# Kernel tuning notes

Measured on AMD Instinct MI355X. Metric: run time of the kernel, lower is better.

The kernel has to match this reference:

```python
import math
import jax, jax.numpy as jnp
import numpy as np

L, H, K, NH, V, DFF = 6, 512, 512, 8, 64, 1024
B, T, S = 8, 512, 512
PAD = 0


def _ln(x, g, b, eps=1e-5):
    m = jnp.mean(x, -1, keepdims=True)
    v = jnp.mean((x - m) ** 2, -1, keepdims=True)
    return (x - m) * jax.lax.rsqrt(v + eps) * g + b


def _mha(Q, Kin, Vin, mask, wq, bq, wk, bk, wv, bv, wo, bo, g, b):
    # weights stored [in, out]
    B_, Tq, Hd = Q.shape
    dk = wq.shape[1] // NH
    dv = wv.shape[1] // NH
    q = (Q @ wq + bq).reshape(B_, Tq, NH, dk).transpose(0, 2, 1, 3)
    k = (Kin @ wk + bk).reshape(B_, -1, NH, dk).transpose(0, 2, 1, 3)
    v = (Vin @ wv + bv).reshape(B_, -1, NH, dv).transpose(0, 2, 1, 3)
    scores = jnp.einsum('bhqd,bhkd->bhqk', q, k) / jnp.sqrt(jnp.float32(dk))
    scores = jnp.where(mask[:, None, :, :], jnp.float32(-1e9), scores)
    attn = jax.nn.softmax(scores, axis=-1)
    ctx = jnp.einsum('bhqk,bhkd->bhqd', attn, v).transpose(0, 2, 1, 3).reshape(B_, Tq, Hd)
    return _ln(ctx @ wo + bo + Q, g, b)


def _pe(t, d):
    pos = jnp.arange(t, dtype=jnp.float32)[:, None]
    div = jnp.exp(jnp.arange(0, d, 2, dtype=jnp.float32) * (-math.log(10000.0) / d))
    pe = jnp.zeros((t, d), jnp.float32)
    pe = pe.at[:, 0::2].set(jnp.sin(pos * div)).at[:, 1::2].set(jnp.cos(pos * div))
    return pe


def setup_inputs() -> dict:
    key = jax.random.key(0)
    ks = iter(jax.random.split(key, 40))
    nrm = lambda shape, s=0.02: jax.random.normal(next(ks), shape, jnp.float32) * s
    inp = {
        'smiles_index': jax.random.randint(next(ks), (B, T), 0, V, dtype=jnp.int32),
        'enc_outputs': jax.random.normal(next(ks), (B, S, H), jnp.float32),
        'enc_pad_mask': jnp.zeros((B, 1, S), bool),
        'tgt_len': T,
        'mol_emb': nrm((V, H), 1.0).at[PAD].set(0.0),  # padding_idx=0 row zeroed
        # self-attn stacks [L, ...]
        'sa_wq': nrm((L, H, K)), 'sa_bq': jnp.zeros((L, K)),
        'sa_wk': nrm((L, H, K)), 'sa_bk': jnp.zeros((L, K)),
        'sa_wv': nrm((L, H, H)), 'sa_bv': jnp.zeros((L, H)),
        'sa_wo': nrm((L, H, H)), 'sa_bo': jnp.zeros((L, H)),
        'ln1_g': jnp.ones((L, H)), 'ln1_b': jnp.zeros((L, H)),
        # cross-attn stacks
        'ea_wq': nrm((L, H, K)), 'ea_bq': jnp.zeros((L, K)),
        'ea_wk': nrm((L, H, K)), 'ea_bk': jnp.zeros((L, K)),
        'ea_wv': nrm((L, H, H)), 'ea_bv': jnp.zeros((L, H)),
        'ea_wo': nrm((L, H, H)), 'ea_bo': jnp.zeros((L, H)),
        'ln2_g': jnp.ones((L, H)), 'ln2_b': jnp.zeros((L, H)),
        # conv1x1 FFN == per-position linear
        'c1_w': nrm((L, H, DFF)), 'c1_b': jnp.zeros((L, DFF)),
        'c2_w': nrm((L, DFF, H)), 'c2_b': jnp.zeros((L, H)),
        'ln3_g': jnp.ones((L, H)), 'ln3_b': jnp.zeros((L, H)),
    }
    return inp


def reference(smiles_index, enc_outputs, enc_pad_mask, tgt_len, mol_emb,
              sa_wq, sa_bq, sa_wk, sa_bk, sa_wv, sa_bv, sa_wo, sa_bo, ln1_g, ln1_b,
              ea_wq, ea_bq, ea_wk, ea_bk, ea_wv, ea_bv, ea_wo, ea_bo, ln2_g, ln2_b,
              c1_w, c1_b, c2_w, c2_b, ln3_g, ln3_b):
    b, t = smiles_index.shape
    s = enc_outputs.shape[1]
    # embeddings + sinusoidal positional encoding (dropout is identity in eval)
    x = mol_emb[smiles_index] + _pe(t, mol_emb.shape[1])[None]
    # masks: pad (key == pad_id) OR causal upper-triangular
    pad = (smiles_index == PAD)[:, None, :]                 # [B,1,T] -> broadcast over queries
    causal = jnp.triu(jnp.ones((t, t), bool), 1)[None]      # [1,T,T]
    self_mask = pad | causal                                # [B,T,T]
    enc_mask = jnp.broadcast_to(enc_pad_mask, (b, t, s))    # [B,T,S]
    for l in range(L):
        x = _mha(x, x, x, self_mask,
                 sa_wq[l], sa_bq[l], sa_wk[l], sa_bk[l], sa_wv[l], sa_bv[l],
                 sa_wo[l], sa_bo[l], ln1_g[l], ln1_b[l])
        x = _mha(x, enc_outputs, enc_outputs, enc_mask,
                 ea_wq[l], ea_bq[l], ea_wk[l], ea_bk[l], ea_wv[l], ea_bv[l],
                 ea_wo[l], ea_bo[l], ln2_g[l], ln2_b[l])
        h = jax.nn.relu(x @ c1_w[l] + c1_b[l])
        y = h @ c2_w[l] + c2_b[l]
        x = _ln(y + x, ln3_g[l], ln3_b[l])
    return x
```

## Files before the change

kernel.cpp:

```cpp
#include <hip/hip_runtime.h>
#include <hip/hip_bf16.h>
#include <math.h>

#define NL   6
#define HD   512
#define NHD  8
#define DK   64
#define DFFN 1024
#define NB   8
#define TT   512
#define MROWS (NB*TT)
#define SQC  262144

typedef __hip_bfloat16 bf16;
typedef __attribute__((ext_vector_type(8))) short short8v;
typedef __attribute__((ext_vector_type(4))) short short4v;
typedef __attribute__((ext_vector_type(4))) float f32x4;

__device__ __forceinline__ float wave_sum(float v) {
#pragma unroll
  for (int off = 32; off; off >>= 1) v += __shfl_xor(v, off);
  return v;
}
__device__ __forceinline__ unsigned short f2bf(float x) {
  __hip_bfloat16 h = __float2bfloat16(x);
  return *reinterpret_cast<unsigned short*>(&h);
}

struct Srcs8 { const float* s[8]; };
__global__ __launch_bounds__(256)
void wprep8_kernel(Srcs8 srcs, bf16* __restrict__ wt) {
  const int z = blockIdx.z;
  const int which = z & 7, l = z >> 3;
  const long long baseT[8] = {0, 0, 0, 18LL*SQC, 24LL*SQC, 30LL*SQC, 30LL*SQC, 42LL*SQC};
  const long long lstrT[8] = {3LL*SQC, 3LL*SQC, 3LL*SQC, SQC, SQC, 2LL*SQC, 2LL*SQC, SQC};
  const int rowOffT[8] = {0, 512, 1024, 0, 0, 0, 512, 0};

  __shared__ float t[32][33];
  const float* W = srcs.s[which] + (size_t)l * SQC;
  bf16* dst = wt + baseT[which] + (size_t)l * lstrT[which] + (size_t)rowOffT[which] * HD;
  const int n0 = blockIdx.x * 32, k0 = blockIdx.y * 32;
  const int tx = threadIdx.x & 31, ty = threadIdx.x >> 5;
#pragma unroll
  for (int j = 0; j < 4; ++j)
    t[ty + j * 8][tx] = W[(size_t)(k0 + ty + j * 8) * HD + n0 + tx];
  __syncthreads();
#pragma unroll
  for (int j = 0; j < 4; ++j)
    dst[(size_t)(n0 + ty + j * 8) * HD + k0 + tx] = __float2bfloat16(t[tx][ty + j * 8]);
}

__global__ __launch_bounds__(256)
void wprep_kernel(const float* __restrict__ W, bf16* __restrict__ Wt, int Kd, int Nd) {
  __shared__ float t[32][33];
  const size_t src = (size_t)blockIdx.z * Kd * Nd;
  const int n0 = blockIdx.x * 32, k0 = blockIdx.y * 32;
  const int tx = threadIdx.x & 31, ty = threadIdx.x >> 5;
#pragma unroll
  for (int j = 0; j < 4; ++j)
    t[ty + j * 8][tx] = W[src + (size_t)(k0 + ty + j * 8) * Nd + n0 + tx];
  __syncthreads();
#pragma unroll
  for (int j = 0; j < 4; ++j)
    Wt[src + (size_t)(n0 + ty + j * 8) * Kd + k0 + tx] = __float2bfloat16(t[tx][ty + j * 8]);
}

__global__ __launch_bounds__(256)
void bcat2_kernel(const float* __restrict__ b0, const float* __restrict__ b1,
                  const float* __restrict__ b2, const float* __restrict__ c0,
                  const float* __restrict__ c1, float* __restrict__ outS,
                  float* __restrict__ outKV) {
  const int l = blockIdx.x;
  if (blockIdx.y == 0) {
    for (int i = threadIdx.x; i < 1536; i += 256) {
      const int seg = i >> 9, off = i & 511;
      const float* src = seg == 0 ? b0 : (seg == 1 ? b1 : b2);
      outS[(size_t)l * 1536 + i] = src[(size_t)l * 512 + off];
    }
  } else {
    for (int i = threadIdx.x; i < 1024; i += 256) {
      const float* src = (i >> 9) == 0 ? c0 : c1;
      outKV[(size_t)l * 1024 + i] = src[(size_t)l * 512 + (i & 511)];
    }
  }
}

__global__ __launch_bounds__(256)
void cvtbf16_kernel(const float* __restrict__ in, unsigned short* __restrict__ out) {
  const int i = (blockIdx.x * 256 + threadIdx.x) * 4;
  float4 v = *(const float4*)(in + i);
  out[i + 0] = f2bf(v.x); out[i + 1] = f2bf(v.y);
  out[i + 2] = f2bf(v.z); out[i + 3] = f2bf(v.w);
}

__global__ __launch_bounds__(256)
void embed_pe_kernel(const int* __restrict__ idx, const float* __restrict__ emb,
                     float* __restrict__ x, unsigned short* __restrict__ xb) {
  const int row = blockIdx.x;
  const int t = row & (TT - 1);
  const int tok = idx[row];
  const float cdiv = -0.017988946009466842f;
#pragma unroll
  for (int e0 = 0; e0 < 2; ++e0) {
    const int e = threadIdx.x + e0 * 256;
    const float div = __expf((float)(e & ~1) * cdiv);
    const float ang = (float)t * div;
    const float pe = (e & 1) ? cosf(ang) : sinf(ang);
    const float v = emb[(size_t)tok * HD + e] + pe;
    x[(size_t)row * HD + e] = v;
    xb[(size_t)row * HD + e] = f2bf(v);
  }
}

__device__ __forceinline__ void gemm_compute(const char* As, const char* Bs,
                                             int wm, int wn, int lane,
                                             f32x4 (&acc)[2][2]) {
  const int rsw = (lane & 7) << 4;
  const int csel = (lane >> 4) * 16;
  short8v af[2][2], bfr[2][2];
#pragma unroll
  for (int m = 0; m < 2; ++m)
#pragma unroll
    for (int kk = 0; kk < 2; ++kk) {
      const int row = wm * 32 + m * 16 + (lane & 15);
      af[m][kk] = *(const short8v*)(As + row * 128 + ((kk * 64 + csel) ^ rsw));
    }
#pragma unroll
  for (int n = 0; n < 2; ++n)
#pragma unroll
    for (int kk = 0; kk < 2; ++kk) {
      const int row = wn * 32 + n * 16 + (lane & 15);
      bfr[n][kk] = *(const short8v*)(Bs + row * 128 + ((kk * 64 + csel) ^ rsw));
    }
#pragma unroll
  for (int m = 0; m < 2; ++m)
#pragma unroll
    for (int n = 0; n < 2; ++n) {
      acc[m][n] = __builtin_amdgcn_mfma_f32_16x16x32_bf16(af[m][0], bfr[n][0], acc[m][n], 0, 0, 0);
      acc[m][n] = __builtin_amdgcn_mfma_f32_16x16x32_bf16(af[m][1], bfr[n][1], acc[m][n], 0, 0, 0);
    }
}

template<int OUT_BF16, int RELU, int ADDRES>
__device__ __forceinline__
void mgemm_body(const bf16* __restrict__ A, const bf16* __restrict__ Bt,
                const float* __restrict__ bias, const float* __restrict__ res,
                float* __restrict__ Cf, unsigned short* __restrict__ Cb,
                int N, int K, int m0, int n0, char* As, char* Bs) {
  const int tid = threadIdx.x;
  const int w = tid >> 6, lane = tid & 63;
  const int wm = w >> 1, wn = w & 1;

  const int sr = w * 16 + (lane >> 3);
  const int scol = (lane & 7) * 16;
  const int swc = scol ^ ((sr & 7) << 4);
  const bf16* ga0 = A + (size_t)(m0 + sr) * K + (scol >> 1);
  const bf16* ga1 = A + (size_t)(m0 + sr + 8) * K + (scol >> 1);
  const bf16* gb0 = Bt + (size_t)(n0 + sr) * K + (scol >> 1);
  const bf16* gb1 = Bt + (size_t)(n0 + sr + 8) * K + (scol >> 1);
  char* la0 = As + sr * 128 + swc;
  char* la1 = As + (sr + 8) * 128 + swc;
  char* lb0 = Bs + sr * 128 + swc;
  char* lb1 = Bs + (sr + 8) * 128 + swc;

  f32x4 acc[2][2] = {};

  short8v ra0 = *(const short8v*)ga0, ra1 = *(const short8v*)ga1;
  short8v rb0 = *(const short8v*)gb0, rb1 = *(const short8v*)gb1;
  short8v sa0, sa1, sb0, sb1;

  for (int k0 = 0; k0 < K; k0 += 128) {
    __syncthreads();
    *(short8v*)la0 = ra0; *(short8v*)la1 = ra1;
    *(short8v*)lb0 = rb0; *(short8v*)lb1 = rb1;
    __syncthreads();
    sa0 = *(const short8v*)(ga0 + k0 + 64); sa1 = *(const short8v*)(ga1 + k0 + 64);
    sb0 = *(const short8v*)(gb0 + k0 + 64); sb1 = *(const short8v*)(gb1 + k0 + 64);
    gemm_compute(As, Bs, wm, wn, lane, acc);
    __syncthreads();
    *(short8v*)la0 = sa0; *(short8v*)la1 = sa1;
    *(short8v*)lb0 = sb0; *(short8v*)lb1 = sb1;
    __syncthreads();
    if (k0 + 128 < K) {
      ra0 = *(const short8v*)(ga0 + k0 + 128); ra1 = *(const short8v*)(ga1 + k0 + 128);
      rb0 = *(const short8v*)(gb0 + k0 + 128); rb1 = *(const short8v*)(gb1 + k0 + 128);
    }
    gemm_compute(As, Bs, wm, wn, lane, acc);
  }

  const int crow = (lane >> 4) * 4;
  const int ccol = lane & 15;
#pragma unroll
  for (int m = 0; m < 2; ++m)
#pragma unroll
    for (int n = 0; n < 2; ++n) {
      const int gr = m0 + wm * 32 + m * 16 + crow;
      const int gc = n0 + wn * 32 + n * 16 + ccol;
      const float bs = bias[gc];
#pragma unroll
      for (int r = 0; r < 4; ++r) {
        float v = acc[m][n][r] + bs;
        if (RELU) v = fmaxf(v, 0.f);
        if (ADDRES) v += res[(size_t)(gr + r) * N + gc];
        if (OUT_BF16) Cb[(size_t)(gr + r) * N + gc] = f2bf(v);
        else          Cf[(size_t)(gr + r) * N + gc] = v;
      }
    }
}

template<int OUT_BF16, int RELU, int ADDRES>
__global__ __launch_bounds__(256)
void mgemm_kernel(const bf16* __restrict__ A, const bf16* __restrict__ Bt,
                  const float* __restrict__ bias, const float* __restrict__ res,
                  float* __restrict__ Cf, unsigned short* __restrict__ Cb,
                  int N, int K) {
  __shared__ __attribute__((aligned(16))) char As[64 * 128];
  __shared__ __attribute__((aligned(16))) char Bs[64 * 128];
  mgemm_body<OUT_BF16, RELU, ADDRES>(A, Bt, bias, res, Cf, Cb, N, K,
                                     blockIdx.x * 64, blockIdx.y * 64, As, Bs);
}

__global__ __launch_bounds__(256)
void mgemm_cross_kernel(const bf16* __restrict__ A1, const bf16* __restrict__ B1,
                        const float* __restrict__ bias1, unsigned short* __restrict__ C1,
                        const bf16* __restrict__ A2, const bf16* __restrict__ B2,
                        const float* __restrict__ bias2, unsigned short* __restrict__ C2) {
  __shared__ __attribute__((aligned(16))) char As[64 * 128];
  __shared__ __attribute__((aligned(16))) char Bs[64 * 128];
  if (blockIdx.y < 8)
    mgemm_body<1, 0, 0>(A1, B1, bias1, nullptr, nullptr, C1, 512, 512,
                        blockIdx.x * 64, blockIdx.y * 64, As, Bs);
  else
    mgemm_body<1, 0, 0>(A2, B2, bias2, nullptr, nullptr, C2, 1024, 512,
                        blockIdx.x * 64, (blockIdx.y - 8) * 64, As, Bs);
}

template<int CAUSAL>
__global__ __launch_bounds__(512)
void mattn_kernel(const unsigned short* __restrict__ q, const unsigned short* __restrict__ kgl,
                  const unsigned short* __restrict__ vgl, unsigned short* __restrict__ ctx,
                  const int* __restrict__ idx, const unsigned char* __restrict__ emask,
                  int qstride, int kvstride) {
  __shared__ __attribute__((aligned(16))) unsigned short kt[64 * 64];
  __shared__ __attribute__((aligned(16))) unsigned short vt[64 * 64];
  __shared__ __attribute__((aligned(16))) unsigned short pl[8][16 * 64];
  __shared__ float km[64];

  const int bh = blockIdx.x;
  const int b = bh >> 3, h = bh & 7;
  const int tid = threadIdx.x, w = tid >> 6, lane = tid & 63;
  const int l4 = lane & 15, g = lane >> 4;

  int qb_w;
  if (CAUSAL) {
    const int strip = (w < 4) ? blockIdx.y : 7 - blockIdx.y;
    qb_w = strip * 64 + (w & 3) * 16;
  } else {
    qb_w = blockIdx.y * 128 + w * 16;
  }
  const int kvEnd = CAUSAL ? (8 - blockIdx.y) * 64 : TT;

  const unsigned short* qp = q + (size_t)(b * TT + qb_w + l4) * qstride + h * DK + g * 8;
  short8v aq0 = *(const short8v*)qp;
  short8v aq1 = *(const short8v*)(qp + 32);

  const int sr_k = tid >> 3, sc8 = tid & 7;
  const unsigned short* kbp = kgl + (size_t)(b * TT + sr_k) * kvstride + h * DK + sc8 * 8;
  const int k2 = (tid & 31) * 2, d4 = (tid >> 5) * 4;
  const unsigned short* vbp0 = vgl + (size_t)(b * TT + k2) * kvstride + h * DK + d4;
  const unsigned short* vbp1 = vbp0 + kvstride;

  short8v rk = *(const short8v*)kbp;
  short4v rv0 = *(const short4v*)vbp0;
  short4v rv1 = *(const short4v*)vbp1;
  float mreg = 0.f;
  if (tid < 64) {
    const int kp = b * TT + tid;
    mreg = (CAUSAL ? (idx[kp] == 0) : (emask[kp] != 0)) ? -1e9f : 0.f;
  }

  float m_r[4], l_r[4];
  f32x4 acc_o[4];
#pragma unroll
  for (int r = 0; r < 4; ++r) { m_r[r] = -1e30f; l_r[r] = 0.f; }
#pragma unroll
  for (int f = 0; f < 4; ++f) acc_o[f] = (f32x4){0.f, 0.f, 0.f, 0.f};

  for (int kt0 = 0; kt0 < kvEnd; kt0 += 64) {
    __syncthreads();
    if (tid < 64) km[tid] = mreg;
    *(short8v*)((char*)kt + sr_k * 128 + ((sc8 * 16) ^ ((sr_k & 7) << 4))) = rk;
#pragma unroll
    for (int j = 0; j < 4; ++j) {
      const int d = d4 + j;
      const unsigned pk = ((unsigned)(unsigned short)rv0[j]) | (((unsigned)(unsigned short)rv1[j]) << 16);
      *(unsigned*)((char*)vt + d * 128 + ((k2 * 2) ^ ((d & 7) << 4))) = pk;
    }
    __syncthreads();

    if (kt0 + 64 < kvEnd) {
      const size_t off = (size_t)(kt0 + 64) * kvstride;
      rk = *(const short8v*)(kbp + off);
      rv0 = *(const short4v*)(vbp0 + off);
      rv1 = *(const short4v*)(vbp1 + off);
      if (tid < 64) {
        const int kp = b * TT + kt0 + 64 + tid;
        mreg = (CAUSAL ? (idx[kp] == 0) : (emask[kp] != 0)) ? -1e9f : 0.f;
      }
    }

    if (!(CAUSAL && kt0 > qb_w + 15)) {
      const bool diag = CAUSAL && (kt0 + 64 > qb_w);

      f32x4 s4[4];
      __builtin_amdgcn_s_setprio(1);
#pragma unroll
      for (int f = 0; f < 4; ++f) {
        const int krow = f * 16 + l4;
        const int sw = (krow & 7) << 4;
        short8v bk0 = *(const short8v*)((const char*)kt + krow * 128 + ((g * 16) ^ sw));
        short8v bk1 = *(const short8v*)((const char*)kt + krow * 128 + ((64 + g * 16) ^ sw));
        f32x4 a = {};
        a = __builtin_amdgcn_mfma_f32_16x16x32_bf16(aq0, bk0, a, 0, 0, 0);
        a = __builtin_amdgcn_mfma_f32_16x16x32_bf16(aq1, bk1, a, 0, 0, 0);
        s4[f] = a;
      }
      __builtin_amdgcn_s_setprio(0);

      float kmb[4];
#pragma unroll
      for (int f = 0; f < 4; ++f) kmb[f] = km[f * 16 + l4];

      float sc_r[4];
#pragma unroll
      for (int r = 0; r < 4; ++r) {
        const int qpos = qb_w + g * 4 + r;
        float sf[4];
#pragma unroll
        for (int f = 0; f < 4; ++f) sf[f] = fmaf(s4[f][r], 0.125f, kmb[f]);
        if (diag) {
#pragma unroll
          for (int f = 0; f < 4; ++f) {
            const int kpos = kt0 + f * 16 + l4;
            sf[f] = (kpos > qpos) ? -1e9f : sf[f];
          }
        }
        float mx = fmaxf(fmaxf(sf[0], sf[1]), fmaxf(sf[2], sf[3]));
#pragma unroll
        for (int off = 8; off; off >>= 1) mx = fmaxf(mx, __shfl_xor(mx, off));
        const float mn = fmaxf(m_r[r], mx);
        const float sc = __expf(m_r[r] - mn);
        m_r[r] = mn;
        sc_r[r] = sc;
        float ps = 0.f;
        const int prow = g * 4 + r;
        const int psw = (prow & 7) << 4;
#pragma unroll
        for (int f = 0; f < 4; ++f) {
          const float p = __expf(sf[f] - mn);
          ps += p;
          *(unsigned short*)((char*)pl[w] + prow * 128 + ((f * 32 + l4 * 2) ^ psw)) = f2bf(p);
        }
#pragma unroll
        for (int off = 8; off; off >>= 1) ps += __shfl_xor(ps, off);
        l_r[r] = l_r[r] * sc + ps;
      }

#pragma unroll
      for (int f = 0; f < 4; ++f)
#pragma unroll
        for (int r = 0; r < 4; ++r) acc_o[f][r] *= sc_r[r];

      const int asw = (l4 & 7) << 4;
      short8v pa0 = *(const short8v*)((const char*)pl[w] + l4 * 128 + ((g * 16) ^ asw));
      short8v pa1 = *(const short8v*)((const char*)pl[w] + l4 * 128 + ((g * 16 + 64) ^ asw));
      __builtin_amdgcn_s_setprio(1);
#pragma unroll
      for (int f = 0; f < 4; ++f) {
        const int drow = f * 16 + l4;
        const int sw = (drow & 7) << 4;
        short8v vb0 = *(const short8v*)((const char*)vt + drow * 128 + ((g * 16) ^ sw));
        short8v vb1 = *(const short8v*)((const char*)vt + drow * 128 + ((g * 16 + 64) ^ sw));
        acc_o[f] = __builtin_amdgcn_mfma_f32_16x16x32_bf16(pa0, vb0, acc_o[f], 0, 0, 0);
        acc_o[f] = __builtin_amdgcn_mfma_f32_16x16x32_bf16(pa1, vb1, acc_o[f], 0, 0, 0);
      }
      __builtin_amdgcn_s_setprio(0);
    }
  }

  float rl[4];
#pragma unroll
  for (int r = 0; r < 4; ++r) rl[r] = 1.f / l_r[r];
#pragma unroll
  for (int f = 0; f < 4; ++f)
#pragma unroll
    for (int r = 0; r < 4; ++r) {
      const int row = qb_w + g * 4 + r;
      const int col = h * DK + f * 16 + l4;
      ctx[(size_t)(b * TT + row) * HD + col] = f2bf(acc_o[f][r] * rl[r]);
    }
}

__global__ __launch_bounds__(256)
void ln2_kernel(const float* __restrict__ v, float* __restrict__ out,
                unsigned short* __restrict__ outb,
                const float* __restrict__ g, const float* __restrict__ bta) {
  const int row = blockIdx.x;
  const int tid = threadIdx.x;
  const int w = tid >> 6, lane = tid & 63;
  const size_t ro = (size_t)row * HD;

  float v0 = v[ro + tid];
  float v1 = v[ro + tid + 256];

  __shared__ float red[4];
  float s = wave_sum(v0 + v1);
  if (lane == 0) red[w] = s;
  __syncthreads();
  const float mean = (red[0] + red[1] + red[2] + red[3]) * (1.f / HD);
  __syncthreads();

  const float d0 = v0 - mean, d1 = v1 - mean;
  float qv = wave_sum(d0 * d0 + d1 * d1);
  if (lane == 0) red[w] = qv;
  __syncthreads();
  const float var = (red[0] + red[1] + red[2] + red[3]) * (1.f / HD);
  const float rstd = rsqrtf(var + 1e-5f);

  const float o0 = d0 * rstd * g[tid] + bta[tid];
  const float o1 = d1 * rstd * g[tid + 256] + bta[tid + 256];
  out[ro + tid] = o0;
  out[ro + tid + 256] = o1;
  outb[ro + tid] = f2bf(o0);
  outb[ro + tid + 256] = f2bf(o1);
}

extern "C" void kernel_launch(void* const* d_in, const int* in_sizes, int n_in,
                              void* d_out, int out_size, void* d_ws, size_t ws_size,
                              hipStream_t stream) {
  const int* idx = (const int*)d_in[0];
  const float* enc = (const float*)d_in[1];
  const unsigned char* emask = (const unsigned char*)d_in[2];
  const float* emb = (const float*)d_in[4];
  const float* sa_wq = (const float*)d_in[5];
  const float* sa_bq = (const float*)d_in[6];
  const float* sa_wk = (const float*)d_in[7];
  const float* sa_bk = (const float*)d_in[8];
  const float* sa_wv = (const float*)d_in[9];
  const float* sa_bv = (const float*)d_in[10];
  const float* sa_wo = (const float*)d_in[11];
  const float* sa_bo = (const float*)d_in[12];
  const float* ln1g = (const float*)d_in[13];
  const float* ln1b = (const float*)d_in[14];
  const float* ea_wq = (const float*)d_in[15];
  const float* ea_bq = (const float*)d_in[16];
  const float* ea_wk = (const float*)d_in[17];
  const float* ea_bk = (const float*)d_in[18];
  const float* ea_wv = (const float*)d_in[19];
  const float* ea_bv = (const float*)d_in[20];
  const float* ea_wo = (const float*)d_in[21];
  const float* ea_bo = (const float*)d_in[22];
  const float* ln2g = (const float*)d_in[23];
  const float* ln2b = (const float*)d_in[24];
  const float* c1w = (const float*)d_in[25];
  const float* c1b = (const float*)d_in[26];
  const float* c2w = (const float*)d_in[27];
  const float* c2b = (const float*)d_in[28];
  const float* ln3g = (const float*)d_in[29];
  const float* ln3b = (const float*)d_in[30];

  const size_t MH = (size_t)MROWS * HD;
  const size_t SQ = (size_t)SQC;
  char* ws = (char*)d_ws;
  float*          x    = (float*)(ws + 0);
  unsigned short* xb   = (unsigned short*)(ws + (8u << 20));
  unsigned short* qkvb = (unsigned short*)(ws + (12u << 20));
  unsigned short* qcb  = (unsigned short*)(ws + (24u << 20));
  unsigned short* kvb  = (unsigned short*)(ws + (28u << 20));
  unsigned short* cxb  = (unsigned short*)(ws + (36u << 20));
  float*          yb   = (float*)(ws + (40u << 20));
  unsigned short* encb = (unsigned short*)(ws + (56u << 20));
  bf16*           wt   = (bf16*)(ws + (60u << 20));
  float*          bcS  = (float*)(ws + (98u << 20));
  float*          bcKV = (float*)(ws + (99u << 20));
  unsigned short* hb   = qkvb;

  bf16* t_saqkv = wt;
  bf16* t_sao   = wt + 18 * SQ;
  bf16* t_eaq   = wt + 24 * SQ;
  bf16* t_eakv  = wt + 30 * SQ;
  bf16* t_eao   = wt + 42 * SQ;
  bf16* t_c1    = wt + 48 * SQ;
  bf16* t_c2    = wt + 60 * SQ;

  const dim3 blk(256);
  const dim3 blk512(512);
  const dim3 gQKV(MROWS / 64, 1536 / 64);
  const dim3 g1024(MROWS / 64, 1024 / 64);
  const dim3 g512(MROWS / 64, 512 / 64);
  const dim3 gCross(MROWS / 64, 24);
  const dim3 attng(NB * NHD, 4);

  Srcs8 s8;
  s8.s[0] = sa_wq; s8.s[1] = sa_wk; s8.s[2] = sa_wv; s8.s[3] = sa_wo;
  s8.s[4] = ea_wq; s8.s[5] = ea_wk; s8.s[6] = ea_wv; s8.s[7] = ea_wo;
  wprep8_kernel<<<dim3(16, 16, 48), blk, 0, stream>>>(s8, wt);
  wprep_kernel<<<dim3(32, 16, NL), blk, 0, stream>>>(c1w, t_c1, HD, DFFN);
  wprep_kernel<<<dim3(16, 32, NL), blk, 0, stream>>>(c2w, t_c2, DFFN, HD);
  bcat2_kernel<<<dim3(NL, 2), blk, 0, stream>>>(sa_bq, sa_bk, sa_bv, ea_bk, ea_bv, bcS, bcKV);
  cvtbf16_kernel<<<MH / 1024, blk, 0, stream>>>(enc, encb);

  embed_pe_kernel<<<MROWS, blk, 0, stream>>>(idx, emb, x, xb);

  for (int l = 0; l < NL; ++l) {
    const size_t b512 = (size_t)l * HD;
    const size_t bFF = (size_t)l * DFFN;
    float* lnout = (l == NL - 1) ? (float*)d_out : x;

    mgemm_kernel<1, 0, 0><<<gQKV, blk, 0, stream>>>(
        (const bf16*)xb, t_saqkv + (size_t)l * 3 * SQ, bcS + (size_t)l * 1536,
        nullptr, nullptr, qkvb, 1536, HD);
    mattn_kernel<1><<<attng, blk512, 0, stream>>>(qkvb, qkvb + 512, qkvb + 1024, cxb,
                                                  idx, emask, 1536, 1536);
    mgemm_kernel<0, 0, 1><<<g512, blk, 0, stream>>>(
        (const bf16*)cxb, t_sao + (size_t)l * SQ, sa_bo + b512, x, yb, nullptr, HD, HD);
    ln2_kernel<<<MROWS, blk, 0, stream>>>(yb, x, xb, ln1g + b512, ln1b + b512);

    mgemm_cross_kernel<<<gCross, blk, 0, stream>>>(
        (const bf16*)xb, t_eaq + (size_t)l * SQ, ea_bq + b512, qcb,
        (const bf16*)encb, t_eakv + (size_t)l * 2 * SQ, bcKV + (size_t)l * 1024, kvb);
    mattn_kernel<0><<<attng, blk512, 0, stream>>>(qcb, kvb, kvb + 512, cxb,
                                                  idx, emask, 512, 1024);
    mgemm_kernel<0, 0, 1><<<g512, blk, 0, stream>>>(
        (const bf16*)cxb, t_eao + (size_t)l * SQ, ea_bo + b512, x, yb, nullptr, HD, HD);
    ln2_kernel<<<MROWS, blk, 0, stream>>>(yb, x, xb, ln2g + b512, ln2b + b512);

    mgemm_kernel<1, 1, 0><<<g1024, blk, 0, stream>>>(
        (const bf16*)xb, t_c1 + (size_t)l * 2 * SQ, c1b + bFF, nullptr, nullptr, hb, DFFN, HD);
    mgemm_kernel<0, 0, 1><<<g512, blk, 0, stream>>>(
        (const bf16*)hb, t_c2 + (size_t)l * 2 * SQ, c2b + b512, x, yb, nullptr, HD, DFFN);
    ln2_kernel<<<MROWS, blk, 0, stream>>>(yb, lnout, xb, ln3g + b512, ln3b + b512);
  }
}
```

Before: 825.2 us.

## Double-buffer LDS tiles in GEMM and attention, add XCD-aware block swizzle

The GEMM and attention kernels now use two LDS buffers for their tiles, which cuts each k-step to a single barrier instead of two. The next tile's global loads are issued before that barrier. Block indices are also remapped so consecutive tiles land on the same XCD, aiming for better L2 reuse across the chiplets. In exchange, LDS use doubles, which may lower occupancy. The swizzle assumes the grid size divides evenly by 8.

```diff
diff --git a/kernel.cpp b/kernel.cpp
--- a/kernel.cpp
+++ b/kernel.cpp
@@ -25,6 +25,13 @@
 __device__ __forceinline__ unsigned short f2bf(float x) {
   __hip_bfloat16 h = __float2bfloat16(x);
   return *reinterpret_cast<unsigned short*>(&h);
+}
+
+__device__ __forceinline__ void xcd_swz(int gy, int& mblk, int& nblk) {
+  const int raw = blockIdx.x * gy + blockIdx.y;
+  const int chunk = (gridDim.x * gy) >> 3;
+  const int swz = (raw & 7) * chunk + (raw >> 3);
+  mblk = swz / gy; nblk = swz % gy;
 }
 
 struct Srcs8 { const float* s[8]; };
@@ -158,34 +165,28 @@
   const bf16* ga1 = A + (size_t)(m0 + sr + 8) * K + (scol >> 1);
   const bf16* gb0 = Bt + (size_t)(n0 + sr) * K + (scol >> 1);
   const bf16* gb1 = Bt + (size_t)(n0 + sr + 8) * K + (scol >> 1);
-  char* la0 = As + sr * 128 + swc;
-  char* la1 = As + (sr + 8) * 128 + swc;
-  char* lb0 = Bs + sr * 128 + swc;
-  char* lb1 = Bs + (sr + 8) * 128 + swc;
 
   f32x4 acc[2][2] = {};
 
   short8v ra0 = *(const short8v*)ga0, ra1 = *(const short8v*)ga1;
   short8v rb0 = *(const short8v*)gb0, rb1 = *(const short8v*)gb1;
-  short8v sa0, sa1, sb0, sb1;
-
-  for (int k0 = 0; k0 < K; k0 += 128) {
+
+  const int NT = K >> 6;
+  for (int t = 0; t < NT; ++t) {
+    char* Ab = As + (t & 1) * 8192;
+    char* Bb = Bs + (t & 1) * 8192;
+    *(short8v*)(Ab + sr * 128 + swc) = ra0;
+    *(short8v*)(Ab + (sr + 8) * 128 + swc) = ra1;
+    *(short8v*)(Bb + sr * 128 + swc) = rb0;
+    *(short8v*)(Bb + (sr + 8) * 128 + swc) = rb1;
+    if (t + 1 < NT) {
+      ra0 = *(const short8v*)(ga0 + (t + 1) * 64);
+      ra1 = *(const short8v*)(ga1 + (t + 1) * 64);
+      rb0 = *(const short8v*)(gb0 + (t + 1) * 64);
+      rb1 = *(const short8v*)(gb1 + (t + 1) * 64);
+    }
     __syncthreads();
-    *(short8v*)la0 = ra0; *(short8v*)la1 = ra1;
-    *(short8v*)lb0 = rb0; *(short8v*)lb1 = rb1;
-    __syncthreads();
-    sa0 = *(const short8v*)(ga0 + k0 + 64); sa1 = *(const short8v*)(ga1 + k0 + 64);
-    sb0 = *(const short8v*)(gb0 + k0 + 64); sb1 = *(const short8v*)(gb1 + k0 + 64);
-    gemm_compute(As, Bs, wm, wn, lane, acc);
-    __syncthreads();
-    *(short8v*)la0 = sa0; *(short8v*)la1 = sa1;
-    *(short8v*)lb0 = sb0; *(short8v*)lb1 = sb1;
-    __syncthreads();
-    if (k0 + 128 < K) {
-      ra0 = *(const short8v*)(ga0 + k0 + 128); ra1 = *(const short8v*)(ga1 + k0 + 128);
-      rb0 = *(const short8v*)(gb0 + k0 + 128); rb1 = *(const short8v*)(gb1 + k0 + 128);
-    }
-    gemm_compute(As, Bs, wm, wn, lane, acc);
+    gemm_compute(Ab, Bb, wm, wn, lane, acc);
   }
 
   const int crow = (lane >> 4) * 4;
@@ -214,10 +215,12 @@
                   const float* __restrict__ bias, const float* __restrict__ res,
                   float* __restrict__ Cf, unsigned short* __restrict__ Cb,
                   int N, int K) {
-  __shared__ __attribute__((aligned(16))) char As[64 * 128];
-  __shared__ __attribute__((aligned(16))) char Bs[64 * 128];
+  __shared__ __attribute__((aligned(16))) char As[2 * 64 * 128];
+  __shared__ __attribute__((aligned(16))) char Bs[2 * 64 * 128];
+  int mblk, nblk;
+  xcd_swz(gridDim.y, mblk, nblk);
   mgemm_body<OUT_BF16, RELU, ADDRES>(A, Bt, bias, res, Cf, Cb, N, K,
-                                     blockIdx.x * 64, blockIdx.y * 64, As, Bs);
+                                     mblk * 64, nblk * 64, As, Bs);
 }
 
 __global__ __launch_bounds__(256)
@@ -225,14 +228,16 @@
                         const float* __restrict__ bias1, unsigned short* __restrict__ C1,
                         const bf16* __restrict__ A2, const bf16* __restrict__ B2,
                         const float* __restrict__ bias2, unsigned short* __restrict__ C2) {
-  __shared__ __attribute__((aligned(16))) char As[64 * 128];
-  __shared__ __attribute__((aligned(16))) char Bs[64 * 128];
-  if (blockIdx.y < 8)
+  __shared__ __attribute__((aligned(16))) char As[2 * 64 * 128];
+  __shared__ __attribute__((aligned(16))) char Bs[2 * 64 * 128];
+  int mblk, nblk;
+  xcd_swz(gridDim.y, mblk, nblk);
+  if (nblk < 8)
     mgemm_body<1, 0, 0>(A1, B1, bias1, nullptr, nullptr, C1, 512, 512,
-                        blockIdx.x * 64, blockIdx.y * 64, As, Bs);
+                        mblk * 64, nblk * 64, As, Bs);
   else
     mgemm_body<1, 0, 0>(A2, B2, bias2, nullptr, nullptr, C2, 1024, 512,
-                        blockIdx.x * 64, (blockIdx.y - 8) * 64, As, Bs);
+                        mblk * 64, (nblk - 8) * 64, As, Bs);
 }
 
 template<int CAUSAL>
@@ -241,24 +246,26 @@
                   const unsigned short* __restrict__ vgl, unsigned short* __restrict__ ctx,
                   const int* __restrict__ idx, const unsigned char* __restrict__ emask,
                   int qstride, int kvstride) {
-  __shared__ __attribute__((aligned(16))) unsigned short kt[64 * 64];
-  __shared__ __attribute__((aligned(16))) unsigned short vt[64 * 64];
+  __shared__ __attribute__((aligned(16))) unsigned short kt[2][64 * 64];
+  __shared__ __attribute__((aligned(16))) unsigned short vt[2][64 * 64];
   __shared__ __attribute__((aligned(16))) unsigned short pl[8][16 * 64];
-  __shared__ float km[64];
-
-  const int bh = blockIdx.x;
+  __shared__ float km[2][64];
+
+  const int raw = blockIdx.x * 4 + blockIdx.y;
+  const int swzid = (raw & 7) * 32 + (raw >> 3);
+  const int bh = swzid >> 2, ybs = swzid & 3;
   const int b = bh >> 3, h = bh & 7;
   const int tid = threadIdx.x, w = tid >> 6, lane = tid & 63;
   const int l4 = lane & 15, g = lane >> 4;
 
   int qb_w;
   if (CAUSAL) {
-    const int strip = (w < 4) ? blockIdx.y : 7 - blockIdx.y;
+    const int strip = (w < 4) ? ybs : 7 - ybs;
     qb_w = strip * 64 + (w & 3) * 16;
   } else {
-    qb_w = blockIdx.y * 128 + w * 16;
-  }
-  const int kvEnd = CAUSAL ? (8 - blockIdx.y) * 64 : TT;
+    qb_w = ybs * 128 + w * 16;
+  }
+  const int kvEnd = CAUSAL ? (8 - ybs) * 64 : TT;
 
   const unsigned short* qp = q + (size_t)(b * TT + qb_w + l4) * qstride + h * DK + g * 8;
   short8v aq0 = *(const short8v*)qp;
@@ -286,18 +293,17 @@
 #pragma unroll
   for (int f = 0; f < 4; ++f) acc_o[f] = (f32x4){0.f, 0.f, 0.f, 0.f};
 
-  for (int kt0 = 0; kt0 < kvEnd; kt0 += 64) {
-    __syncthreads();
-    if (tid < 64) km[tid] = mreg;
-    *(short8v*)((char*)kt + sr_k * 128 + ((sc8 * 16) ^ ((sr_k & 7) << 4))) = rk;
+  int tix = 0;
+  for (int kt0 = 0; kt0 < kvEnd; kt0 += 64, ++tix) {
+    const int buf = tix & 1;
+    if (tid < 64) km[buf][tid] = mreg;
+    *(short8v*)((char*)kt[buf] + sr_k * 128 + ((sc8 * 16) ^ ((sr_k & 7) << 4))) = rk;
 #pragma unroll
     for (int j = 0; j < 4; ++j) {
       const int d = d4 + j;
       const unsigned pk = ((unsigned)(unsigned short)rv0[j]) | (((unsigned)(unsigned short)rv1[j]) << 16);
-      *(unsigned*)((char*)vt + d * 128 + ((k2 * 2) ^ ((d & 7) << 4))) = pk;
-    }
-    __syncthreads();
-
+      *(unsigned*)((char*)vt[buf] + d * 128 + ((k2 * 2) ^ ((d & 7) << 4))) = pk;
+    }
     if (kt0 + 64 < kvEnd) {
       const size_t off = (size_t)(kt0 + 64) * kvstride;
       rk = *(const short8v*)(kbp + off);
@@ -308,6 +314,7 @@
         mreg = (CAUSAL ? (idx[kp] == 0) : (emask[kp] != 0)) ? -1e9f : 0.f;
       }
     }
+    __syncthreads();
 
     if (!(CAUSAL && kt0 > qb_w + 15)) {
       const bool diag = CAUSAL && (kt0 + 64 > qb_w);
@@ -318,8 +325,8 @@
       for (int f = 0; f < 4; ++f) {
         const int krow = f * 16 + l4;
         const int sw = (krow & 7) << 4;
-        short8v bk0 = *(const short8v*)((const char*)kt + krow * 128 + ((g * 16) ^ sw));
-        short8v bk1 = *(const short8v*)((const char*)kt + krow * 128 + ((64 + g * 16) ^ sw));
+        short8v bk0 = *(const short8v*)((const char*)kt[buf] + krow * 128 + ((g * 16) ^ sw));
+        short8v bk1 = *(const short8v*)((const char*)kt[buf] + krow * 128 + ((64 + g * 16) ^ sw));
         f32x4 a = {};
         a = __builtin_amdgcn_mfma_f32_16x16x32_bf16(aq0, bk0, a, 0, 0, 0);
         a = __builtin_amdgcn_mfma_f32_16x16x32_bf16(aq1, bk1, a, 0, 0, 0);
@@ -329,7 +336,7 @@
 
       float kmb[4];
 #pragma unroll
-      for (int f = 0; f < 4; ++f) kmb[f] = km[f * 16 + l4];
+      for (int f = 0; f < 4; ++f) kmb[f] = km[buf][f * 16 + l4];
 
       float sc_r[4];
 #pragma unroll
@@ -379,8 +386,8 @@
       for (int f = 0; f < 4; ++f) {
         const int drow = f * 16 + l4;
         const int sw = (drow & 7) << 4;
-        short8v vb0 = *(const short8v*)((const char*)vt + drow * 128 + ((g * 16) ^ sw));
-        short8v vb1 = *(const short8v*)((const char*)vt + drow * 128 + ((g * 16 + 64) ^ sw));
+        short8v vb0 = *(const short8v*)((const char*)vt[buf] + drow * 128 + ((g * 16) ^ sw));
+        short8v vb1 = *(const short8v*)((const char*)vt[buf] + drow * 128 + ((g * 16 + 64) ^ sw));
         acc_o[f] = __builtin_amdgcn_mfma_f32_16x16x32_bf16(pa0, vb0, acc_o[f], 0, 0, 0);
         acc_o[f] = __builtin_amdgcn_mfma_f32_16x16x32_bf16(pa1, vb1, acc_o[f], 0, 0, 0);
       }
```

Result: no change. 841.3 us (+2.0%).

## Stream GEMM tiles directly into double-buffered LDS with async global loads

Applied to the files above, without the earlier changes.

Replaces the register-staged GEMM main loop with `global_load_lds` transfers that write 16-byte chunks straight from global memory into LDS, using a double buffer. The next K-tile is issued while the current one is computed, and there is one barrier per tile instead of four per 128-wide step. The XOR swizzle is preserved by permuting which global chunk each lane fetches. This doubles GEMM shared memory and depends on the async loads completing before the barrier, which the code does not wait for explicitly.

```diff
diff --git a/kernel.cpp b/kernel.cpp
--- a/kernel.cpp
+++ b/kernel.cpp
@@ -25,6 +25,12 @@
 __device__ __forceinline__ unsigned short f2bf(float x) {
   __hip_bfloat16 h = __float2bfloat16(x);
   return *reinterpret_cast<unsigned short*>(&h);
+}
+
+__device__ __forceinline__ void gload16(const void* g, void* l) {
+  __builtin_amdgcn_global_load_lds(
+      (const __attribute__((address_space(1))) unsigned int*)g,
+      (__attribute__((address_space(3))) unsigned int*)l, 16, 0, 0);
 }
 
 struct Srcs8 { const float* s[8]; };
@@ -150,42 +156,31 @@
   const int tid = threadIdx.x;
   const int w = tid >> 6, lane = tid & 63;
   const int wm = w >> 1, wn = w & 1;
-
-  const int sr = w * 16 + (lane >> 3);
-  const int scol = (lane & 7) * 16;
-  const int swc = scol ^ ((sr & 7) << 4);
-  const bf16* ga0 = A + (size_t)(m0 + sr) * K + (scol >> 1);
-  const bf16* ga1 = A + (size_t)(m0 + sr + 8) * K + (scol >> 1);
-  const bf16* gb0 = Bt + (size_t)(n0 + sr) * K + (scol >> 1);
-  const bf16* gb1 = Bt + (size_t)(n0 + sr + 8) * K + (scol >> 1);
-  char* la0 = As + sr * 128 + swc;
-  char* la1 = As + (sr + 8) * 128 + swc;
-  char* lb0 = Bs + sr * 128 + swc;
-  char* lb1 = Bs + (sr + 8) * 128 + swc;
+  const int lrow = lane >> 3;
+  const int lchk = (lane & 7) ^ lrow;
+
+  const bf16* ga0 = A + (size_t)(m0 + w * 16 + lrow) * K + lchk * 8;
+  const bf16* ga1 = ga0 + (size_t)8 * K;
+  const bf16* gb0 = Bt + (size_t)(n0 + w * 16 + lrow) * K + lchk * 8;
+  const bf16* gb1 = gb0 + (size_t)8 * K;
 
   f32x4 acc[2][2] = {};
-
-  short8v ra0 = *(const short8v*)ga0, ra1 = *(const short8v*)ga1;
-  short8v rb0 = *(const short8v*)gb0, rb1 = *(const short8v*)gb1;
-  short8v sa0, sa1, sb0, sb1;
-
-  for (int k0 = 0; k0 < K; k0 += 128) {
+  const int NT = K >> 6;
+
+  auto issue = [&](int t, int buf) {
+    char* Ab = As + buf * 8192;
+    char* Bb = Bs + buf * 8192;
+    gload16(ga0 + t * 64, Ab + (w * 16) * 128);
+    gload16(ga1 + t * 64, Ab + (w * 16 + 8) * 128);
+    gload16(gb0 + t * 64, Bb + (w * 16) * 128);
+    gload16(gb1 + t * 64, Bb + (w * 16 + 8) * 128);
+  };
+
+  issue(0, 0);
+  for (int t = 0; t < NT; ++t) {
     __syncthreads();
-    *(short8v*)la0 = ra0; *(short8v*)la1 = ra1;
-    *(short8v*)lb0 = rb0; *(short8v*)lb1 = rb1;
-    __syncthreads();
-    sa0 = *(const short8v*)(ga0 + k0 + 64); sa1 = *(const short8v*)(ga1 + k0 + 64);
-    sb0 = *(const short8v*)(gb0 + k0 + 64); sb1 = *(const short8v*)(gb1 + k0 + 64);
-    gemm_compute(As, Bs, wm, wn, lane, acc);
-    __syncthreads();
-    *(short8v*)la0 = sa0; *(short8v*)la1 = sa1;
-    *(short8v*)lb0 = sb0; *(short8v*)lb1 = sb1;
-    __syncthreads();
-    if (k0 + 128 < K) {
-      ra0 = *(const short8v*)(ga0 + k0 + 128); ra1 = *(const short8v*)(ga1 + k0 + 128);
-      rb0 = *(const short8v*)(gb0 + k0 + 128); rb1 = *(const short8v*)(gb1 + k0 + 128);
-    }
-    gemm_compute(As, Bs, wm, wn, lane, acc);
+    if (t + 1 < NT) issue(t + 1, (t + 1) & 1);
+    gemm_compute(As + (t & 1) * 8192, Bs + (t & 1) * 8192, wm, wn, lane, acc);
   }
 
   const int crow = (lane >> 4) * 4;
@@ -214,8 +209,8 @@
                   const float* __restrict__ bias, const float* __restrict__ res,
                   float* __restrict__ Cf, unsigned short* __restrict__ Cb,
                   int N, int K) {
-  __shared__ __attribute__((aligned(16))) char As[64 * 128];
-  __shared__ __attribute__((aligned(16))) char Bs[64 * 128];
+  __shared__ __attribute__((aligned(16))) char As[2 * 64 * 128];
+  __shared__ __attribute__((aligned(16))) char Bs[2 * 64 * 128];
   mgemm_body<OUT_BF16, RELU, ADDRES>(A, Bt, bias, res, Cf, Cb, N, K,
                                      blockIdx.x * 64, blockIdx.y * 64, As, Bs);
 }
@@ -225,8 +220,8 @@
                         const float* __restrict__ bias1, unsigned short* __restrict__ C1,
                         const bf16* __restrict__ A2, const bf16* __restrict__ B2,
                         const float* __restrict__ bias2, unsigned short* __restrict__ C2) {
-  __shared__ __attribute__((aligned(16))) char As[64 * 128];
-  __shared__ __attribute__((aligned(16))) char Bs[64 * 128];
+  __shared__ __attribute__((aligned(16))) char As[2 * 64 * 128];
+  __shared__ __attribute__((aligned(16))) char Bs[2 * 64 * 128];
   if (blockIdx.y < 8)
     mgemm_body<1, 0, 0>(A1, B1, bias1, nullptr, nullptr, C1, 512, 512,
                         blockIdx.x * 64, blockIdx.y * 64, As, Bs);
```

New measurement: 848.9 us. 2.9% more time.

## Precompute all-layer cross-attention K/V upfront and store residual-sum in bf16

Applied to the files above, without the earlier changes.

Cross-attention K/V projections depend only on the encoder outputs, so they are now computed for all six layers in one large GEMM launch before the layer loop. This replaces the per-layer combined Q+KV cross kernel with a plain Q GEMM. Separately, the residual-added pre-LayerNorm sum is written as bf16 instead of fp32, which halves the traffic between the output-projection GEMMs and the LayerNorm kernel. The trade-offs are a larger workspace holding KV for every layer and some extra rounding error before each LayerNorm.

```diff
diff --git a/kernel.cpp b/kernel.cpp
--- a/kernel.cpp
+++ b/kernel.cpp
@@ -25,6 +25,9 @@
 __device__ __forceinline__ unsigned short f2bf(float x) {
   __hip_bfloat16 h = __float2bfloat16(x);
   return *reinterpret_cast<unsigned short*>(&h);
+}
+__device__ __forceinline__ float bf2f(unsigned short u) {
+  return __uint_as_float(((unsigned)u) << 16);
 }
 
 struct Srcs8 { const float* s[8]; };
@@ -221,18 +224,14 @@
 }
 
 __global__ __launch_bounds__(256)
-void mgemm_cross_kernel(const bf16* __restrict__ A1, const bf16* __restrict__ B1,
-                        const float* __restrict__ bias1, unsigned short* __restrict__ C1,
-                        const bf16* __restrict__ A2, const bf16* __restrict__ B2,
-                        const float* __restrict__ bias2, unsigned short* __restrict__ C2) {
+void mgemm_eakv_kernel(const bf16* __restrict__ A, const bf16* __restrict__ BtBase,
+                       const float* __restrict__ biasBase, unsigned short* __restrict__ CBase) {
   __shared__ __attribute__((aligned(16))) char As[64 * 128];
   __shared__ __attribute__((aligned(16))) char Bs[64 * 128];
-  if (blockIdx.y < 8)
-    mgemm_body<1, 0, 0>(A1, B1, bias1, nullptr, nullptr, C1, 512, 512,
-                        blockIdx.x * 64, blockIdx.y * 64, As, Bs);
-  else
-    mgemm_body<1, 0, 0>(A2, B2, bias2, nullptr, nullptr, C2, 1024, 512,
-                        blockIdx.x * 64, (blockIdx.y - 8) * 64, As, Bs);
+  const int l = blockIdx.y >> 4, ny = blockIdx.y & 15;
+  mgemm_body<1, 0, 0>(A, BtBase + (size_t)l * 2 * SQC, biasBase + (size_t)l * 1024,
+                      nullptr, nullptr, CBase + (size_t)l * MROWS * 1024,
+                      1024, 512, blockIdx.x * 64, ny * 64, As, Bs);
 }
 
 template<int CAUSAL>
@@ -402,7 +401,7 @@
 }
 
 __global__ __launch_bounds__(256)
-void ln2_kernel(const float* __restrict__ v, float* __restrict__ out,
+void ln2_kernel(const unsigned short* __restrict__ v, float* __restrict__ out,
                 unsigned short* __restrict__ outb,
                 const float* __restrict__ g, const float* __restrict__ bta) {
   const int row = blockIdx.x;
@@ -410,8 +409,8 @@
   const int w = tid >> 6, lane = tid & 63;
   const size_t ro = (size_t)row * HD;
 
-  float v0 = v[ro + tid];
-  float v1 = v[ro + tid + 256];
+  float v0 = bf2f(v[ro + tid]);
+  float v1 = bf2f(v[ro + tid + 256]);
 
   __shared__ float red[4];
   float s = wave_sum(v0 + v1);
@@ -476,13 +475,13 @@
   unsigned short* xb   = (unsigned short*)(ws + (8u << 20));
   unsigned short* qkvb = (unsigned short*)(ws + (12u << 20));
   unsigned short* qcb  = (unsigned short*)(ws + (24u << 20));
-  unsigned short* kvb  = (unsigned short*)(ws + (28u << 20));
-  unsigned short* cxb  = (unsigned short*)(ws + (36u << 20));
-  float*          yb   = (float*)(ws + (40u << 20));
-  unsigned short* encb = (unsigned short*)(ws + (56u << 20));
-  bf16*           wt   = (bf16*)(ws + (60u << 20));
-  float*          bcS  = (float*)(ws + (98u << 20));
-  float*          bcKV = (float*)(ws + (99u << 20));
+  unsigned short* cxb  = (unsigned short*)(ws + (28u << 20));
+  unsigned short* ybb  = (unsigned short*)(ws + (32u << 20));
+  unsigned short* encb = (unsigned short*)(ws + (36u << 20));
+  bf16*           wt   = (bf16*)(ws + (40u << 20));
+  float*          bcS  = (float*)(ws + (78u << 20));
+  float*          bcKV = (float*)(ws + (79u << 20));
+  unsigned short* kvb6 = (unsigned short*)(ws + (80u << 20));
   unsigned short* hb   = qkvb;
 
   bf16* t_saqkv = wt;
@@ -498,7 +497,7 @@
   const dim3 gQKV(MROWS / 64, 1536 / 64);
   const dim3 g1024(MROWS / 64, 1024 / 64);
   const dim3 g512(MROWS / 64, 512 / 64);
-  const dim3 gCross(MROWS / 64, 24);
+  const dim3 gEAKV(MROWS / 64, 96);
   const dim3 attng(NB * NHD, 4);
 
   Srcs8 s8;
@@ -509,6 +508,7 @@
   wprep_kernel<<<dim3(16, 32, NL), blk, 0, stream>>>(c2w, t_c2, DFFN, HD);
   bcat2_kernel<<<dim3(NL, 2), blk, 0, stream>>>(sa_bq, sa_bk, sa_bv, ea_bk, ea_bv, bcS, bcKV);
   cvtbf16_kernel<<<MH / 1024, blk, 0, stream>>>(enc, encb);
+  mgemm_eakv_kernel<<<gEAKV, blk, 0, stream>>>((const bf16*)encb, t_eakv, bcKV, kvb6);
 
   embed_pe_kernel<<<MROWS, blk, 0, stream>>>(idx, emb, x, xb);
 
@@ -516,29 +516,29 @@
     const size_t b512 = (size_t)l * HD;
     const size_t bFF = (size_t)l * DFFN;
     float* lnout = (l == NL - 1) ? (float*)d_out : x;
+    unsigned short* kvl = kvb6 + (size_t)l * MROWS * 1024;
 
     mgemm_kernel<1, 0, 0><<<gQKV, blk, 0, stream>>>(
         (const bf16*)xb, t_saqkv + (size_t)l * 3 * SQ, bcS + (size_t)l * 1536,
         nullptr, nullptr, qkvb, 1536, HD);
     mattn_kernel<1><<<attng, blk512, 0, stream>>>(qkvb, qkvb + 512, qkvb + 1024, cxb,
                                                   idx, emask, 1536, 1536);
-    mgemm_kernel<0, 0, 1><<<g512, blk, 0, stream>>>(
-        (const bf16*)cxb, t_sao + (size_t)l * SQ, sa_bo + b512, x, yb, nullptr, HD, HD);
-    ln2_kernel<<<MROWS, blk, 0, stream>>>(yb, x, xb, ln1g + b512, ln1b + b512);
-
-    mgemm_cross_kernel<<<gCross, blk, 0, stream>>>(
-        (const bf16*)xb, t_eaq + (size_t)l * SQ, ea_bq + b512, qcb,
-        (const bf16*)encb, t_eakv + (size_t)l * 2 * SQ, bcKV + (size_t)l * 1024, kvb);
-    mattn_kernel<0><<<attng, blk512, 0, stream>>>(qcb, kvb, kvb + 512, cxb,
+    mgemm_kernel<1, 0, 1><<<g512, blk, 0, stream>>>(
+        (const bf16*)cxb, t_sao + (size_t)l * SQ, sa_bo + b512, x, nullptr, ybb, HD, HD);
+    ln2_kernel<<<MROWS, blk, 0, stream>>>(ybb, x, xb, ln1g + b512, ln1b + b512);
+
+    mgemm_kernel<1, 0, 0><<<g512, blk, 0, stream>>>(
+        (const bf16*)xb, t_eaq + (size_t)l * SQ, ea_bq + b512, nullptr, nullptr, qcb, HD, HD);
+    mattn_kernel<0><<<attng, blk512, 0, stream>>>(qcb, kvl, kvl + 512, cxb,
                                                   idx, emask, 512, 1024);
-    mgemm_kernel<0, 0, 1><<<g512, blk, 0, stream>>>(
-        (const bf16*)cxb, t_eao + (size_t)l * SQ, ea_bo + b512, x, yb, nullptr, HD, HD);
-    ln2_kernel<<<MROWS, blk, 0, stream>>>(yb, x, xb, ln2g + b512, ln2b + b512);
+    mgemm_kernel<1, 0, 1><<<g512, blk, 0, stream>>>(
+        (const bf16*)cxb, t_eao + (size_t)l * SQ, ea_bo + b512, x, nullptr, ybb, HD, HD);
+    ln2_kernel<<<MROWS, blk, 0, stream>>>(ybb, x, xb, ln2g + b512, ln2b + b512);
 
     mgemm_kernel<1, 1, 0><<<g1024, blk, 0, stream>>>(
         (const bf16*)xb, t_c1 + (size_t)l * 2 * SQ, c1b + bFF, nullptr, nullptr, hb, DFFN, HD);
-    mgemm_kernel<0, 0, 1><<<g512, blk, 0, stream>>>(
-        (const bf16*)hb, t_c2 + (size_t)l * 2 * SQ, c2b + b512, x, yb, nullptr, HD, DFFN);
-    ln2_kernel<<<MROWS, blk, 0, stream>>>(yb, lnout, xb, ln3g + b512, ln3b + b512);
-  }
-}
+    mgemm_kernel<1, 0, 1><<<g512, blk, 0, stream>>>(
+        (const bf16*)hb, t_c2 + (size_t)l * 2 * SQ, c2b + b512, x, nullptr, ybb, HD, DFFN);
+    ln2_kernel<<<MROWS, blk, 0, stream>>>(ybb, lnout, xb, ln3g + b512, ln3b + b512);
+  }
+}
```

Result: no change. 820.0 us (-0.6%).
